# Kernel optimization log

Hardware: AMD Instinct MI355X
Metric: run time of the kernel (lower is better)

The kernel has to match this reference:

```python
import jax, jax.numpy as jnp
import numpy as np

# ---- model constants (match init_kwargs) ----
NX, NY, H, K, GRID = 32, 1, 64, 3, 5
MID = 2 * H + 1            # 129, middle width of each KAN block
NB = GRID + K              # 8 B-spline basis functions per edge
BATCH = 65536


def _grid_pts():
    # uniform extended grid on [-1, 1] with K extra knots each side: GRID+2K+1 pts
    step = 2.0 / GRID
    return jnp.arange(-K, GRID + K + 1, dtype=jnp.float32) * step - 1.0


def bspline_basis(x):
    """Cox-de Boor B-spline bases. x: [B, I] -> [B, I, GRID+K]."""
    g = _grid_pts()[None, None, :]          # [1,1,P]
    xe = x[..., None]                       # [B,I,1]
    B0 = ((xe >= g[..., :-1]) & (xe < g[..., 1:])).astype(x.dtype)
    Bp = B0
    for p in range(1, K + 1):
        left = (xe - g[..., :-(p + 1)]) / (g[..., p:-1] - g[..., :-(p + 1)])
        right = (g[..., p + 1:] - xe) / (g[..., p + 1:] - g[..., 1:-p])
        Bp = left * Bp[..., :-1] + right * Bp[..., 1:]
    return Bp  # [B, I, NB]


def kan_layer(x, coef, sb, ss, bias):
    """pykan KANLayer: y_o = sum_i sb[i,o]*silu(x_i) + ss[i,o]*spline_io(x_i) + bias_o.
    x: [B,I]; coef: [I,O,NB]; sb, ss: [I,O]; bias: [O]."""
    bs = bspline_basis(x)                                   # [B,I,NB]
    spline = jnp.einsum('bip,iop->bo', bs, coef * ss[:, :, None])
    return jax.nn.silu(x) @ sb + spline + bias


def setup_inputs() -> dict:
    key = jax.random.key(0)
    ks = iter(jax.random.split(key, 40))

    def xavier(k, shape, fan_in, fan_out):
        gain = np.sqrt(2.0)  # relu gain, as in the torch module
        std = gain * np.sqrt(2.0 / (fan_in + fan_out))
        return (std * jax.random.normal(k, shape, dtype=jnp.float32))

    inp = {
        'x': jax.random.normal(next(ks), (BATCH, NX), dtype=jnp.float32),
        'W_in': xavier(next(ks), (NX, H), NX, H),
        'b_in': jnp.zeros((H,), jnp.float32),
        'W_out': xavier(next(ks), (H, NY), H, NY),
    }
    for l in range(2):  # num_hidden_layers KAN blocks, each = 2 KANLayers
        for tag, (din, dout) in [('a', (H, MID)), ('b', (MID, H))]:
            inp[f'coef{l}{tag}'] = xavier(next(ks), (din, dout, NB), din * NB, dout)
            inp[f'sb{l}{tag}'] = xavier(next(ks), (din, dout), din, dout)
            inp[f'ss{l}{tag}'] = jnp.ones((din, dout), jnp.float32)
            inp[f'bias{l}{tag}'] = jnp.zeros((dout,), jnp.float32)
    return inp


def reference(x, W_in, b_in, W_out,
              coef0a, sb0a, ss0a, bias0a, coef0b, sb0b, ss0b, bias0b,
              coef1a, sb1a, ss1a, bias1a, coef1b, sb1b, ss1b, bias1b):
    h = jax.nn.relu(x @ W_in + b_in)
    for (ca, sa, ta, ba, cb, sbb, tb, bb) in (
        (coef0a, sb0a, ss0a, bias0a, coef0b, sb0b, ss0b, bias0b),
        (coef1a, sb1a, ss1a, bias1a, coef1b, sb1b, ss1b, bias1b),
    ):
        h = kan_layer(h, ca, sa, ta, ba)   # H -> 2H+1
        h = kan_layer(h, cb, sbb, tb, bb)  # 2H+1 -> H
    return jax.nn.sigmoid(h @ W_out)       # [B, NY]
```

## Files before the change

### kernel.cpp

```cpp
#include <hip/hip_runtime.h>
#include <math.h>
#include <stdint.h>

#define BATCH 65536
#define TB 128

typedef __fp16   fp16x2  __attribute__((ext_vector_type(2)));
typedef _Float16 half8   __attribute__((ext_vector_type(8)));
typedef float    floatx16 __attribute__((ext_vector_type(16)));

#define SH 68
#define SM 130
#define HM_SLICE (32*SM + 64)

#define WIN 2048
#define KSA 36
#define KSB 74
#define WA (KSA*5*512)
#define WB (KSB*2*512)
#define WTOT (WIN + 2*(WA+WB))

__global__ void setup_weights(
    const float* __restrict__ W_in,
    const float* __restrict__ c0a, const float* __restrict__ sb0a, const float* __restrict__ ss0a,
    const float* __restrict__ c0b, const float* __restrict__ sb0b, const float* __restrict__ ss0b,
    const float* __restrict__ c1a, const float* __restrict__ sb1a, const float* __restrict__ ss1a,
    const float* __restrict__ c1b, const float* __restrict__ sb1b, const float* __restrict__ ss1b,
    _Float16* __restrict__ wt) {
  int idx = blockIdx.x * 256 + threadIdx.x;
  if (idx >= WTOT) return;
  float v = 0.0f;
  if (idx < WIN) {
    int ks = idx >> 10; int nt = (idx >> 9) & 1;
    int q = idx & 511;  int l = q >> 3;   int j = q & 7;
    int n = nt*32 + (l & 31);
    int k = ks*16 + (l >> 5)*8 + j;
    v = W_in[k*64 + n];
  } else {
    int e2   = idx - WIN;
    int pair = (e2 >= WA + WB) ? 1 : 0;
    int e    = e2 - pair * (WA + WB);
    if (e < WA) {
      const float* coef = pair ? c1a : c0a;
      const float* sb   = pair ? sb1a : sb0a;
      const float* ss   = pair ? ss1a : ss0a;
      int ks = e / 2560; int r = e - ks*2560;
      int nt = r >> 9;   int q = r & 511;
      int l  = q >> 3;   int j = q & 7;
      int n  = nt*32 + (l & 31);
      int k  = ks*16 + (l >> 5)*8 + j;
      if (n < 129) {
        if (k < 512) { int i = k >> 3, p = k & 7; v = ss[i*129+n] * coef[(i*129+n)*8 + p]; }
        else         { int i = k - 512; if (i < 64) v = sb[i*129+n]; }
      }
    } else {
      const float* coef = pair ? c1b : c0b;
      const float* sb   = pair ? sb1b : sb0b;
      const float* ss   = pair ? ss1b : ss0b;
      int eb = e - WA;
      int ks = eb >> 10; int r = eb & 1023;
      int nt = r >> 9;   int q = r & 511;
      int l  = q >> 3;   int j = q & 7;
      int n  = nt*32 + (l & 31);
      int k  = ks*16 + (l >> 5)*8 + j;
      if (k < 1032)      { int i = k >> 3, p = k & 7; v = ss[i*64+n] * coef[(i*64+n)*8 + p]; }
      else if (k >= 1040){ int s = k - 1040; if (s < 129) v = sb[s*64+n]; }
    }
  }
  wt[idx] = (_Float16)v;
}

__device__ __forceinline__ half8 feat8(float x) {
  float s  = fmaf(x, 2.5f, 5.5f);
  float mf = floorf(s);
  int   m  = (int)mf;
  float u  = s - mf;
  float t  = 1.0f - u;
  float u2 = u*u;
  float t2 = t*t;
  float w0 = t2 * (t * (1.0f/6.0f));
  float w3 = u2 * (u * (1.0f/6.0f));
  float w1 = fmaf(u2, fmaf(0.5f, u, -1.0f), 2.0f/3.0f);
  float w2 = fmaf(t2, fmaf(0.5f, t, -1.0f), 2.0f/3.0f);
  union { fp16x2 h2[2]; uint64_t u64; } P;
  P.h2[0] = __builtin_amdgcn_cvt_pkrtz(w0, w1);
  P.h2[1] = __builtin_amdgcn_cvt_pkrtz(w2, w3);
  uint64_t T = ((unsigned)m <= 10u) ? P.u64 : 0ull;
  int A = (m << 4) - 48;
  uint64_t L  = T << (A & 63);
  uint64_t R_ = T >> ((-A) & 63);
  uint64_t q0 = (A >= 0) ? ((A < 64) ? L : 0ull) : R_;
  uint64_t q1 = (A >= 64) ? L : ((A > 0) ? R_ : 0ull);
  union { uint64_t q[2]; half8 h; } R;
  R.q[0] = q0; R.q[1] = q1;
  return R.h;
}

__device__ __forceinline__ float extract_half(uint32_t w, int khs) {
  union { uint32_t u; _Float16 h[2]; } cv;
  cv.u = w >> khs;
  return (float)cv.h[0];
}

__device__ __forceinline__ float silu(float x) {
  return x * __builtin_amdgcn_rcpf(1.0f + __expf(-x));
}

template<int KSPL, int KSIL, int NT, int SIN, int O, int SOUT>
__device__ __forceinline__ void kan_layer(
    const _Float16* __restrict__ hinw, _Float16* __restrict__ houtw,
    const _Float16* __restrict__ wt, const float* __restrict__ bias, int lane) {
  constexpr int KTOT = KSPL + KSIL;
  constexpr int NG   = KSPL / 8;
  constexpr int KR   = KSPL - NG*8;
  static_assert(KR == 0 || KR == 1, "remainder must be 0/1");
  const int ln  = lane & 31;
  const int kh  = lane >> 5;
  const int khs = kh << 4;
  const half8* __restrict__ bp = (const half8*)wt + lane;
  floatx16 acc[NT];
  #pragma unroll
  for (int j = 0; j < NT; ++j)
    #pragma unroll
    for (int e = 0; e < 16; ++e) acc[j][e] = 0.0f;

  half8 B[2][NT];
  #pragma unroll
  for (int d = 0; d < 2; ++d)
    #pragma unroll
    for (int j = 0; j < NT; ++j) B[d][j] = bp[(d*NT + j)*64];

  union H8 { half8 h; uint32_t d[4]; };

  #pragma unroll 1
  for (int g = 0; g < NG; ++g) {
    H8 ha, hb;
    ha.h = *(const half8*)&hinw[ln*SIN + g*16];
    hb.h = *(const half8*)&hinw[ln*SIN + g*16 + 8];
    #pragma unroll
    for (int u = 0; u < 8; ++u) {
      uint32_t w = (u < 4) ? ha.d[u] : hb.d[u & 3];
      half8 A = feat8(extract_half(w, khs));
      #pragma unroll
      for (int j = 0; j < NT; ++j)
        acc[j] = __builtin_amdgcn_mfma_f32_32x32x16_f16(A, B[u & 1][j], acc[j], 0, 0, 0);
      #pragma unroll
      for (int j = 0; j < NT; ++j)
        B[u & 1][j] = bp[((g*8 + u + 2)*NT + j)*64];
    }
  }

  if (KR == 1) {
    constexpr int ks = NG*8;
    H8 hc;
    hc.h = *(const half8*)&hinw[ln*SIN + ks*2];
    half8 A = feat8(extract_half(hc.d[0], khs));
    #pragma unroll
    for (int j = 0; j < NT; ++j)
      acc[j] = __builtin_amdgcn_mfma_f32_32x32x16_f16(A, B[ks & 1][j], acc[j], 0, 0, 0);
    #pragma unroll
    for (int j = 0; j < NT; ++j)
      B[ks & 1][j] = bp[((ks + 2)*NT + j)*64];
  }

  #pragma unroll
  for (int sk = 0; sk < KSIL; ++sk) {
    const int ks = KSPL + sk;
    half8 h8 = *(const half8*)&hinw[ln*SIN + sk*16 + kh*8];
    union { fp16x2 h2[4]; half8 v; } Au;
    #pragma unroll
    for (int e = 0; e < 4; ++e) {
      float s0 = silu((float)h8[2*e]);
      float s1 = silu((float)h8[2*e + 1]);
      Au.h2[e] = __builtin_amdgcn_cvt_pkrtz(s0, s1);
    }
    #pragma unroll
    for (int j = 0; j < NT; ++j)
      acc[j] = __builtin_amdgcn_mfma_f32_32x32x16_f16(Au.v, B[ks & 1][j], acc[j], 0, 0, 0);
    const int nks = (ks + 2 < KTOT) ? (ks + 2) : (KTOT - 1);
    #pragma unroll
    for (int j = 0; j < NT; ++j)
      B[ks & 1][j] = bp[(nks*NT + j)*64];
  }

  #pragma unroll
  for (int j = 0; j < NT; ++j) {
    int col = j*32 + ln;
    if (col < O) {
      float bv = bias[col];
      #pragma unroll
      for (int r = 0; r < 16; ++r) {
        int row = (r & 3) + 8*(r >> 2) + 4*kh;
        houtw[row*SOUT + col] = (_Float16)(acc[j][r] + bv);
      }
    }
  }
}

extern "C" __global__ void __launch_bounds__(256, 2)
kan_forward(const float* __restrict__ x, const float* __restrict__ b_in,
            const float* __restrict__ W_out, const _Float16* __restrict__ wt,
            const float* __restrict__ bias0a, const float* __restrict__ bias0b,
            const float* __restrict__ bias1a, const float* __restrict__ bias1b,
            float* __restrict__ out) {
  __shared__ _Float16 hM[4][HM_SLICE];
  __shared__ _Float16 hH[4][32*SH];
  const int t    = threadIdx.x;
  const int wv   = t >> 6;
  const int lane = t & 63;
  const int ln   = lane & 31;
  const int kh   = lane >> 5;
  _Float16* hMw = hM[wv];
  _Float16* hHw = hH[wv];
  const int rbase = blockIdx.x * TB + wv * 32;

  hMw[32*SM + lane] = (_Float16)0.0f;
  if (lane < 32) hMw[lane*SM + 129] = (_Float16)0.0f;

  {
    const float* xr = &x[(rbase + ln)*32 + kh*8];
    float4 v0 = *(const float4*)&xr[0];
    float4 v1 = *(const float4*)&xr[4];
    float4 v2 = *(const float4*)&xr[16];
    float4 v3 = *(const float4*)&xr[20];
    union { fp16x2 h2[4]; half8 h8; } A0, A1;
    A0.h2[0] = __builtin_amdgcn_cvt_pkrtz(v0.x, v0.y);
    A0.h2[1] = __builtin_amdgcn_cvt_pkrtz(v0.z, v0.w);
    A0.h2[2] = __builtin_amdgcn_cvt_pkrtz(v1.x, v1.y);
    A0.h2[3] = __builtin_amdgcn_cvt_pkrtz(v1.z, v1.w);
    A1.h2[0] = __builtin_amdgcn_cvt_pkrtz(v2.x, v2.y);
    A1.h2[1] = __builtin_amdgcn_cvt_pkrtz(v2.z, v2.w);
    A1.h2[2] = __builtin_amdgcn_cvt_pkrtz(v3.x, v3.y);
    A1.h2[3] = __builtin_amdgcn_cvt_pkrtz(v3.z, v3.w);
    const half8* bp = (const half8*)wt + lane;
    #pragma unroll
    for (int nt = 0; nt < 2; ++nt) {
      floatx16 a;
      #pragma unroll
      for (int e = 0; e < 16; ++e) a[e] = 0.0f;
      a = __builtin_amdgcn_mfma_f32_32x32x16_f16(A0.h8, bp[nt*64],       a, 0, 0, 0);
      a = __builtin_amdgcn_mfma_f32_32x32x16_f16(A1.h8, bp[(2 + nt)*64], a, 0, 0, 0);
      int col = nt*32 + ln;
      float bv = b_in[col];
      #pragma unroll
      for (int r = 0; r < 16; ++r) {
        int row = (r & 3) + 8*(r >> 2) + 4*kh;
        hHw[row*SH + col] = (_Float16)fmaxf(a[r] + bv, 0.0f);
      }
    }
  }

  kan_layer<32,4,5,SH,129,SM>(hHw, hMw, wt + WIN,             bias0a, lane);
  kan_layer<65,9,2,SM, 64,SH>(hMw, hHw, wt + WIN + WA,        bias0b, lane);
  kan_layer<32,4,5,SH,129,SM>(hHw, hMw, wt + WIN + WA + WB,   bias1a, lane);
  kan_layer<65,9,2,SM, 64,SH>(hMw, hHw, wt + WIN + 2*WA + WB, bias1b, lane);

  {
    float s = 0.0f;
    #pragma unroll
    for (int j = 0; j < 32; ++j)
      s = fmaf((float)hHw[ln*SH + kh*32 + j], W_out[kh*32 + j], s);
    s += __shfl_down(s, 32);
    if (lane < 32)
      out[rbase + ln] = __builtin_amdgcn_rcpf(1.0f + __expf(-s));
  }
}

extern "C" void kernel_launch(void* const* d_in, const int* in_sizes, int n_in,
                              void* d_out, int out_size, void* d_ws, size_t ws_size,
                              hipStream_t stream) {
  const float* x     = (const float*)d_in[0];
  const float* W_in  = (const float*)d_in[1];
  const float* b_in  = (const float*)d_in[2];
  const float* W_out = (const float*)d_in[3];
  const float* c0a = (const float*)d_in[4];  const float* sb0a = (const float*)d_in[5];
  const float* ss0a= (const float*)d_in[6];  const float* bias0a=(const float*)d_in[7];
  const float* c0b = (const float*)d_in[8];  const float* sb0b = (const float*)d_in[9];
  const float* ss0b= (const float*)d_in[10]; const float* bias0b=(const float*)d_in[11];
  const float* c1a = (const float*)d_in[12]; const float* sb1a = (const float*)d_in[13];
  const float* ss1a= (const float*)d_in[14]; const float* bias1a=(const float*)d_in[15];
  const float* c1b = (const float*)d_in[16]; const float* sb1b = (const float*)d_in[17];
  const float* ss1b= (const float*)d_in[18]; const float* bias1b=(const float*)d_in[19];
  float*    out = (float*)d_out;
  _Float16* wt  = (_Float16*)d_ws;

  setup_weights<<<(WTOT + 255)/256, 256, 0, stream>>>(
      W_in, c0a, sb0a, ss0a, c0b, sb0b, ss0b,
      c1a, sb1a, ss1a, c1b, sb1b, ss1b, wt);

  kan_forward<<<BATCH/TB, 256, 0, stream>>>(
      x, b_in, W_out, wt, bias0a, bias0b, bias1a, bias1b, out);
}
```

Measured before the change: 155.0 us.

## Replace analytic cubic B-spline feature expansion with shared-memory lookup table interpolation

Replaces per-element cubic B-spline weight evaluation and 64-bit shift placement with a per-block LDS table. The table holds pre-placed half8 basis vectors for each interval and 64 sub-steps, and values are linearly interpolated in packed fp16. The feature vectors for a group are now computed before the MFMA loop, which separates the VALU work from the matrix ops. This lowers ALU work per feature but adds LDS gathers that may bank-conflict, a table build and __syncthreads per block, and interpolation error in the basis weights.

```diff
diff --git a/kernel.cpp b/kernel.cpp
--- a/kernel.cpp
+++ b/kernel.cpp
@@ -12,6 +12,10 @@
 #define SH 68
 #define SM 130
 #define HM_SLICE (32*SM + 64)
+
+#define FT_ROW 66
+#define FT_ENT (12*FT_ROW)
+#define FT_HALVES (FT_ENT*8)
 
 #define WIN 2048
 #define KSA 36
@@ -70,29 +74,25 @@
   wt[idx] = (_Float16)v;
 }
 
-__device__ __forceinline__ half8 feat8(float x) {
-  float s  = fmaf(x, 2.5f, 5.5f);
-  float mf = floorf(s);
-  int   m  = (int)mf;
-  float u  = s - mf;
-  float t  = 1.0f - u;
-  float u2 = u*u;
-  float t2 = t*t;
-  float w0 = t2 * (t * (1.0f/6.0f));
-  float w3 = u2 * (u * (1.0f/6.0f));
-  float w1 = fmaf(u2, fmaf(0.5f, u, -1.0f), 2.0f/3.0f);
-  float w2 = fmaf(t2, fmaf(0.5f, t, -1.0f), 2.0f/3.0f);
-  union { fp16x2 h2[2]; uint64_t u64; } P;
-  P.h2[0] = __builtin_amdgcn_cvt_pkrtz(w0, w1);
-  P.h2[1] = __builtin_amdgcn_cvt_pkrtz(w2, w3);
-  uint64_t T = ((unsigned)m <= 10u) ? P.u64 : 0ull;
-  int A = (m << 4) - 48;
-  uint64_t L  = T << (A & 63);
-  uint64_t R_ = T >> ((-A) & 63);
-  uint64_t q0 = (A >= 0) ? ((A < 64) ? L : 0ull) : R_;
-  uint64_t q1 = (A >= 64) ? L : ((A > 0) ? R_ : 0ull);
-  union { uint64_t q[2]; half8 h; } R;
-  R.q[0] = q0; R.q[1] = q1;
+__device__ __forceinline__ half8 feat8_t(float x, const _Float16* __restrict__ ftab) {
+  float s   = fmaf(x, 2.5f, 5.5f);
+  float mf  = floorf(s);
+  float u   = s - mf;
+  int   m   = (int)mf;
+  unsigned mm = ((unsigned)m <= 10u) ? (unsigned)m : 11u;
+  float uf  = u * 64.0f;
+  float ubf = floorf(uf);
+  float fr  = uf - ubf;
+  int idx = (int)mm * FT_ROW + (int)ubf;
+  const half8* e = (const half8*)&ftab[idx * 8];
+  union { half8 h; fp16x2 p[4]; } T0, T1, R;
+  T0.h = e[0];
+  T1.h = e[1];
+  __fp16 fh = (__fp16)fr;
+  fp16x2 f2; f2[0] = fh; f2[1] = fh;
+  #pragma unroll
+  for (int i = 0; i < 4; ++i)
+    R.p[i] = T0.p[i] + f2 * (T1.p[i] - T0.p[i]);
   return R.h;
 }
 
@@ -109,7 +109,8 @@
 template<int KSPL, int KSIL, int NT, int SIN, int O, int SOUT>
 __device__ __forceinline__ void kan_layer(
     const _Float16* __restrict__ hinw, _Float16* __restrict__ houtw,
-    const _Float16* __restrict__ wt, const float* __restrict__ bias, int lane) {
+    const _Float16* __restrict__ wt, const float* __restrict__ bias,
+    const _Float16* __restrict__ ftab, int lane) {
   constexpr int KTOT = KSPL + KSIL;
   constexpr int NG   = KSPL / 8;
   constexpr int KR   = KSPL - NG*8;
@@ -137,13 +138,17 @@
     H8 ha, hb;
     ha.h = *(const half8*)&hinw[ln*SIN + g*16];
     hb.h = *(const half8*)&hinw[ln*SIN + g*16 + 8];
+    half8 A[8];
     #pragma unroll
     for (int u = 0; u < 8; ++u) {
       uint32_t w = (u < 4) ? ha.d[u] : hb.d[u & 3];
-      half8 A = feat8(extract_half(w, khs));
+      A[u] = feat8_t(extract_half(w, khs), ftab);
+    }
+    #pragma unroll
+    for (int u = 0; u < 8; ++u) {
       #pragma unroll
       for (int j = 0; j < NT; ++j)
-        acc[j] = __builtin_amdgcn_mfma_f32_32x32x16_f16(A, B[u & 1][j], acc[j], 0, 0, 0);
+        acc[j] = __builtin_amdgcn_mfma_f32_32x32x16_f16(A[u], B[u & 1][j], acc[j], 0, 0, 0);
       #pragma unroll
       for (int j = 0; j < NT; ++j)
         B[u & 1][j] = bp[((g*8 + u + 2)*NT + j)*64];
@@ -152,9 +157,8 @@
 
   if (KR == 1) {
     constexpr int ks = NG*8;
-    H8 hc;
-    hc.h = *(const half8*)&hinw[ln*SIN + ks*2];
-    half8 A = feat8(extract_half(hc.d[0], khs));
+    uint32_t w = *(const uint32_t*)&hinw[ln*SIN + ks*2];
+    half8 A = feat8_t(extract_half(w, khs), ftab);
     #pragma unroll
     for (int j = 0; j < NT; ++j)
       acc[j] = __builtin_amdgcn_mfma_f32_32x32x16_f16(A, B[ks & 1][j], acc[j], 0, 0, 0);
@@ -205,6 +209,7 @@
             float* __restrict__ out) {
   __shared__ _Float16 hM[4][HM_SLICE];
   __shared__ _Float16 hH[4][32*SH];
+  __shared__ __align__(16) _Float16 ftab[FT_HALVES];
   const int t    = threadIdx.x;
   const int wv   = t >> 6;
   const int lane = t & 63;
@@ -214,8 +219,29 @@
   _Float16* hHw = hH[wv];
   const int rbase = blockIdx.x * TB + wv * 32;
 
+  for (int e = t; e < 12*65; e += 256) {
+    int m  = e / 65;
+    int ub = e - m*65;
+    float u  = (float)ub * (1.0f/64.0f);
+    float t1 = 1.0f - u;
+    float w0 = t1*t1*t1*(1.0f/6.0f);
+    float w1 = fmaf(u*u, fmaf(0.5f, u, -1.0f), 2.0f/3.0f);
+    float w2 = fmaf(t1*t1, fmaf(0.5f, t1, -1.0f), 2.0f/3.0f);
+    float w3 = u*u*u*(1.0f/6.0f);
+    float w[4] = {w0, w1, w2, w3};
+    half8 hv;
+    #pragma unroll
+    for (int j = 0; j < 8; ++j) {
+      int k = j - m + 3;
+      float v = (m <= 10 && k >= 0 && k < 4) ? w[k] : 0.0f;
+      hv[j] = (_Float16)v;
+    }
+    *(half8*)&ftab[(m*FT_ROW + ub)*8] = hv;
+  }
+
   hMw[32*SM + lane] = (_Float16)0.0f;
   if (lane < 32) hMw[lane*SM + 129] = (_Float16)0.0f;
+  __syncthreads();
 
   {
     const float* xr = &x[(rbase + ln)*32 + kh*8];
@@ -250,10 +276,10 @@
     }
   }
 
-  kan_layer<32,4,5,SH,129,SM>(hHw, hMw, wt + WIN,             bias0a, lane);
-  kan_layer<65,9,2,SM, 64,SH>(hMw, hHw, wt + WIN + WA,        bias0b, lane);
-  kan_layer<32,4,5,SH,129,SM>(hHw, hMw, wt + WIN + WA + WB,   bias1a, lane);
-  kan_layer<65,9,2,SM, 64,SH>(hMw, hHw, wt + WIN + 2*WA + WB, bias1b, lane);
+  kan_layer<32,4,5,SH,129,SM>(hHw, hMw, wt + WIN,             bias0a, ftab, lane);
+  kan_layer<65,9,2,SM, 64,SH>(hMw, hHw, wt + WIN + WA,        bias0b, ftab, lane);
+  kan_layer<32,4,5,SH,129,SM>(hHw, hMw, wt + WIN + WA + WB,   bias1a, ftab, lane);
+  kan_layer<65,9,2,SM, 64,SH>(hMw, hHw, wt + WIN + 2*WA + WB, bias1b, ftab, lane);
 
   {
     float s = 0.0f;
```

After: 158.0 us. About the same (+1.9%).

## Process two 32-row tiles per wave to reuse B fragments across MFMAs

Applied to the files above, without the earlier changes.

Each wave now handles 64 rows as two 32-row tiles that share every weight (B) fragment loaded from global memory. This halves weight loads per row and interleaves two independent MFMA chains. Blocks shrink to 128 threads (2 waves) with launch bounds of 1 block, so the grid and shared memory per block stay the same. Keeping two accumulator sets (up to 10 floatx16 for NT=5) raises VGPR/AGPR pressure and may cut occupancy or cause spills.

```diff
diff --git a/kernel.cpp b/kernel.cpp
--- a/kernel.cpp
+++ b/kernel.cpp
@@ -107,8 +107,9 @@
 }
 
 template<int KSPL, int KSIL, int NT, int SIN, int O, int SOUT>
-__device__ __forceinline__ void kan_layer(
-    const _Float16* __restrict__ hinw, _Float16* __restrict__ houtw,
+__device__ __forceinline__ void kan_layer2(
+    const _Float16* __restrict__ hin0, const _Float16* __restrict__ hin1,
+    _Float16* __restrict__ hout0, _Float16* __restrict__ hout1,
     const _Float16* __restrict__ wt, const float* __restrict__ bias, int lane) {
   constexpr int KTOT = KSPL + KSIL;
   constexpr int NG   = KSPL / 8;
@@ -118,11 +119,11 @@
   const int kh  = lane >> 5;
   const int khs = kh << 4;
   const half8* __restrict__ bp = (const half8*)wt + lane;
-  floatx16 acc[NT];
+  floatx16 acc0[NT], acc1[NT];
   #pragma unroll
   for (int j = 0; j < NT; ++j)
     #pragma unroll
-    for (int e = 0; e < 16; ++e) acc[j][e] = 0.0f;
+    for (int e = 0; e < 16; ++e) { acc0[j][e] = 0.0f; acc1[j][e] = 0.0f; }
 
   half8 B[2][NT];
   #pragma unroll
@@ -134,16 +135,23 @@
 
   #pragma unroll 1
   for (int g = 0; g < NG; ++g) {
-    H8 ha, hb;
-    ha.h = *(const half8*)&hinw[ln*SIN + g*16];
-    hb.h = *(const half8*)&hinw[ln*SIN + g*16 + 8];
+    H8 ha0, hb0, ha1, hb1;
+    ha0.h = *(const half8*)&hin0[ln*SIN + g*16];
+    hb0.h = *(const half8*)&hin0[ln*SIN + g*16 + 8];
+    ha1.h = *(const half8*)&hin1[ln*SIN + g*16];
+    hb1.h = *(const half8*)&hin1[ln*SIN + g*16 + 8];
     #pragma unroll
     for (int u = 0; u < 8; ++u) {
-      uint32_t w = (u < 4) ? ha.d[u] : hb.d[u & 3];
-      half8 A = feat8(extract_half(w, khs));
+      uint32_t w0 = (u < 4) ? ha0.d[u] : hb0.d[u & 3];
+      uint32_t w1 = (u < 4) ? ha1.d[u] : hb1.d[u & 3];
+      half8 A0 = feat8(extract_half(w0, khs));
+      half8 A1 = feat8(extract_half(w1, khs));
       #pragma unroll
       for (int j = 0; j < NT; ++j)
-        acc[j] = __builtin_amdgcn_mfma_f32_32x32x16_f16(A, B[u & 1][j], acc[j], 0, 0, 0);
+        acc0[j] = __builtin_amdgcn_mfma_f32_32x32x16_f16(A0, B[u & 1][j], acc0[j], 0, 0, 0);
+      #pragma unroll
+      for (int j = 0; j < NT; ++j)
+        acc1[j] = __builtin_amdgcn_mfma_f32_32x32x16_f16(A1, B[u & 1][j], acc1[j], 0, 0, 0);
       #pragma unroll
       for (int j = 0; j < NT; ++j)
         B[u & 1][j] = bp[((g*8 + u + 2)*NT + j)*64];
@@ -152,12 +160,16 @@
 
   if (KR == 1) {
     constexpr int ks = NG*8;
-    H8 hc;
-    hc.h = *(const half8*)&hinw[ln*SIN + ks*2];
-    half8 A = feat8(extract_half(hc.d[0], khs));
-    #pragma unroll
-    for (int j = 0; j < NT; ++j)
-      acc[j] = __builtin_amdgcn_mfma_f32_32x32x16_f16(A, B[ks & 1][j], acc[j], 0, 0, 0);
+    uint32_t w0 = *(const uint32_t*)&hin0[ln*SIN + ks*2];
+    uint32_t w1 = *(const uint32_t*)&hin1[ln*SIN + ks*2];
+    half8 A0 = feat8(extract_half(w0, khs));
+    half8 A1 = feat8(extract_half(w1, khs));
+    #pragma unroll
+    for (int j = 0; j < NT; ++j)
+      acc0[j] = __builtin_amdgcn_mfma_f32_32x32x16_f16(A0, B[ks & 1][j], acc0[j], 0, 0, 0);
+    #pragma unroll
+    for (int j = 0; j < NT; ++j)
+      acc1[j] = __builtin_amdgcn_mfma_f32_32x32x16_f16(A1, B[ks & 1][j], acc1[j], 0, 0, 0);
     #pragma unroll
     for (int j = 0; j < NT; ++j)
       B[ks & 1][j] = bp[((ks + 2)*NT + j)*64];
@@ -166,17 +178,20 @@
   #pragma unroll
   for (int sk = 0; sk < KSIL; ++sk) {
     const int ks = KSPL + sk;
-    half8 h8 = *(const half8*)&hinw[ln*SIN + sk*16 + kh*8];
-    union { fp16x2 h2[4]; half8 v; } Au;
+    half8 h80 = *(const half8*)&hin0[ln*SIN + sk*16 + kh*8];
+    half8 h81 = *(const half8*)&hin1[ln*SIN + sk*16 + kh*8];
+    union { fp16x2 h2[4]; half8 v; } Au0, Au1;
     #pragma unroll
     for (int e = 0; e < 4; ++e) {
-      float s0 = silu((float)h8[2*e]);
-      float s1 = silu((float)h8[2*e + 1]);
-      Au.h2[e] = __builtin_amdgcn_cvt_pkrtz(s0, s1);
-    }
-    #pragma unroll
-    for (int j = 0; j < NT; ++j)
-      acc[j] = __builtin_amdgcn_mfma_f32_32x32x16_f16(Au.v, B[ks & 1][j], acc[j], 0, 0, 0);
+      Au0.h2[e] = __builtin_amdgcn_cvt_pkrtz(silu((float)h80[2*e]), silu((float)h80[2*e + 1]));
+      Au1.h2[e] = __builtin_amdgcn_cvt_pkrtz(silu((float)h81[2*e]), silu((float)h81[2*e + 1]));
+    }
+    #pragma unroll
+    for (int j = 0; j < NT; ++j)
+      acc0[j] = __builtin_amdgcn_mfma_f32_32x32x16_f16(Au0.v, B[ks & 1][j], acc0[j], 0, 0, 0);
+    #pragma unroll
+    for (int j = 0; j < NT; ++j)
+      acc1[j] = __builtin_amdgcn_mfma_f32_32x32x16_f16(Au1.v, B[ks & 1][j], acc1[j], 0, 0, 0);
     const int nks = (ks + 2 < KTOT) ? (ks + 2) : (KTOT - 1);
     #pragma unroll
     for (int j = 0; j < NT; ++j)
@@ -191,78 +206,88 @@
       #pragma unroll
       for (int r = 0; r < 16; ++r) {
         int row = (r & 3) + 8*(r >> 2) + 4*kh;
-        houtw[row*SOUT + col] = (_Float16)(acc[j][r] + bv);
+        hout0[row*SOUT + col] = (_Float16)(acc0[j][r] + bv);
+        hout1[row*SOUT + col] = (_Float16)(acc1[j][r] + bv);
       }
     }
   }
 }
 
-extern "C" __global__ void __launch_bounds__(256, 2)
+extern "C" __global__ void __launch_bounds__(128, 1)
 kan_forward(const float* __restrict__ x, const float* __restrict__ b_in,
             const float* __restrict__ W_out, const _Float16* __restrict__ wt,
             const float* __restrict__ bias0a, const float* __restrict__ bias0b,
             const float* __restrict__ bias1a, const float* __restrict__ bias1b,
             float* __restrict__ out) {
-  __shared__ _Float16 hM[4][HM_SLICE];
-  __shared__ _Float16 hH[4][32*SH];
+  __shared__ _Float16 hM[2][2][HM_SLICE];
+  __shared__ _Float16 hH[2][2][32*SH];
   const int t    = threadIdx.x;
   const int wv   = t >> 6;
   const int lane = t & 63;
   const int ln   = lane & 31;
   const int kh   = lane >> 5;
-  _Float16* hMw = hM[wv];
-  _Float16* hHw = hH[wv];
-  const int rbase = blockIdx.x * TB + wv * 32;
-
-  hMw[32*SM + lane] = (_Float16)0.0f;
-  if (lane < 32) hMw[lane*SM + 129] = (_Float16)0.0f;
+  _Float16* hM0 = hM[wv][0];
+  _Float16* hM1 = hM[wv][1];
+  _Float16* hH0 = hH[wv][0];
+  _Float16* hH1 = hH[wv][1];
+  const int rbase = blockIdx.x * TB + wv * 64;
+
+  hM0[32*SM + lane] = (_Float16)0.0f;
+  hM1[32*SM + lane] = (_Float16)0.0f;
+  if (lane < 32) { hM0[lane*SM + 129] = (_Float16)0.0f; hM1[lane*SM + 129] = (_Float16)0.0f; }
 
   {
-    const float* xr = &x[(rbase + ln)*32 + kh*8];
-    float4 v0 = *(const float4*)&xr[0];
-    float4 v1 = *(const float4*)&xr[4];
-    float4 v2 = *(const float4*)&xr[16];
-    float4 v3 = *(const float4*)&xr[20];
-    union { fp16x2 h2[4]; half8 h8; } A0, A1;
-    A0.h2[0] = __builtin_amdgcn_cvt_pkrtz(v0.x, v0.y);
-    A0.h2[1] = __builtin_amdgcn_cvt_pkrtz(v0.z, v0.w);
-    A0.h2[2] = __builtin_amdgcn_cvt_pkrtz(v1.x, v1.y);
-    A0.h2[3] = __builtin_amdgcn_cvt_pkrtz(v1.z, v1.w);
-    A1.h2[0] = __builtin_amdgcn_cvt_pkrtz(v2.x, v2.y);
-    A1.h2[1] = __builtin_amdgcn_cvt_pkrtz(v2.z, v2.w);
-    A1.h2[2] = __builtin_amdgcn_cvt_pkrtz(v3.x, v3.y);
-    A1.h2[3] = __builtin_amdgcn_cvt_pkrtz(v3.z, v3.w);
     const half8* bp = (const half8*)wt + lane;
     #pragma unroll
-    for (int nt = 0; nt < 2; ++nt) {
-      floatx16 a;
-      #pragma unroll
-      for (int e = 0; e < 16; ++e) a[e] = 0.0f;
-      a = __builtin_amdgcn_mfma_f32_32x32x16_f16(A0.h8, bp[nt*64],       a, 0, 0, 0);
-      a = __builtin_amdgcn_mfma_f32_32x32x16_f16(A1.h8, bp[(2 + nt)*64], a, 0, 0, 0);
-      int col = nt*32 + ln;
-      float bv = b_in[col];
-      #pragma unroll
-      for (int r = 0; r < 16; ++r) {
-        int row = (r & 3) + 8*(r >> 2) + 4*kh;
-        hHw[row*SH + col] = (_Float16)fmaxf(a[r] + bv, 0.0f);
+    for (int tt = 0; tt < 2; ++tt) {
+      const float* xr = &x[(size_t)(rbase + tt*32 + ln)*32 + kh*8];
+      float4 v0 = *(const float4*)&xr[0];
+      float4 v1 = *(const float4*)&xr[4];
+      float4 v2 = *(const float4*)&xr[16];
+      float4 v3 = *(const float4*)&xr[20];
+      union { fp16x2 h2[4]; half8 h8; } A0, A1;
+      A0.h2[0] = __builtin_amdgcn_cvt_pkrtz(v0.x, v0.y);
+      A0.h2[1] = __builtin_amdgcn_cvt_pkrtz(v0.z, v0.w);
+      A0.h2[2] = __builtin_amdgcn_cvt_pkrtz(v1.x, v1.y);
+      A0.h2[3] = __builtin_amdgcn_cvt_pkrtz(v1.z, v1.w);
+      A1.h2[0] = __builtin_amdgcn_cvt_pkrtz(v2.x, v2.y);
+      A1.h2[1] = __builtin_amdgcn_cvt_pkrtz(v2.z, v2.w);
+      A1.h2[2] = __builtin_amdgcn_cvt_pkrtz(v3.x, v3.y);
+      A1.h2[3] = __builtin_amdgcn_cvt_pkrtz(v3.z, v3.w);
+      _Float16* hHt = (tt == 0) ? hH0 : hH1;
+      #pragma unroll
+      for (int nt = 0; nt < 2; ++nt) {
+        floatx16 a;
+        #pragma unroll
+        for (int e = 0; e < 16; ++e) a[e] = 0.0f;
+        a = __builtin_amdgcn_mfma_f32_32x32x16_f16(A0.h8, bp[nt*64],       a, 0, 0, 0);
+        a = __builtin_amdgcn_mfma_f32_32x32x16_f16(A1.h8, bp[(2 + nt)*64], a, 0, 0, 0);
+        int col = nt*32 + ln;
+        float bv = b_in[col];
+        #pragma unroll
+        for (int r = 0; r < 16; ++r) {
+          int row = (r & 3) + 8*(r >> 2) + 4*kh;
+          hHt[row*SH + col] = (_Float16)fmaxf(a[r] + bv, 0.0f);
+        }
       }
     }
   }
 
-  kan_layer<32,4,5,SH,129,SM>(hHw, hMw, wt + WIN,             bias0a, lane);
-  kan_layer<65,9,2,SM, 64,SH>(hMw, hHw, wt + WIN + WA,        bias0b, lane);
-  kan_layer<32,4,5,SH,129,SM>(hHw, hMw, wt + WIN + WA + WB,   bias1a, lane);
-  kan_layer<65,9,2,SM, 64,SH>(hMw, hHw, wt + WIN + 2*WA + WB, bias1b, lane);
-
-  {
+  kan_layer2<32,4,5,SH,129,SM>(hH0, hH1, hM0, hM1, wt + WIN,             bias0a, lane);
+  kan_layer2<65,9,2,SM, 64,SH>(hM0, hM1, hH0, hH1, wt + WIN + WA,        bias0b, lane);
+  kan_layer2<32,4,5,SH,129,SM>(hH0, hH1, hM0, hM1, wt + WIN + WA + WB,   bias1a, lane);
+  kan_layer2<65,9,2,SM, 64,SH>(hM0, hM1, hH0, hH1, wt + WIN + 2*WA + WB, bias1b, lane);
+
+  #pragma unroll
+  for (int tt = 0; tt < 2; ++tt) {
+    const _Float16* hHt = (tt == 0) ? hH0 : hH1;
     float s = 0.0f;
     #pragma unroll
     for (int j = 0; j < 32; ++j)
-      s = fmaf((float)hHw[ln*SH + kh*32 + j], W_out[kh*32 + j], s);
+      s = fmaf((float)hHt[ln*SH + kh*32 + j], W_out[kh*32 + j], s);
     s += __shfl_down(s, 32);
     if (lane < 32)
-      out[rbase + ln] = __builtin_amdgcn_rcpf(1.0f + __expf(-s));
+      out[rbase + tt*32 + ln] = __builtin_amdgcn_rcpf(1.0f + __expf(-s));
   }
 }
 
@@ -288,6 +313,6 @@
       W_in, c0a, sb0a, ss0a, c0b, sb0b, ss0b,
       c1a, sb1a, ss1a, c1b, sb1b, ss1b, wt);
 
-  kan_forward<<<BATCH/TB, 256, 0, stream>>>(
+  kan_forward<<<BATCH/TB, 128, 0, stream>>>(
       x, b_in, W_out, wt, bias0a, bias0b, bias1a, bias1b, out);
 }
```

New measurement: 160.1 us. +3.3%, slower.
